# Kernel optimization log

Measured on AMD Instinct MI355X. Metric: run time of the kernel, lower is better.

The kernel has to match this reference:

```python
import jax, jax.numpy as jnp
import numpy as np

N_NODES = 50000
N_EDGES = 600000
N_GRAPHS = 256
N_FL1, N_MPL, N_FL2, N_FL3 = 128, 128, 128, 64
EPS = 1e-12


def _glorot(key, shape):
    lim = float(np.sqrt(6.0 / (shape[0] + shape[1])))
    return jax.random.uniform(key, shape, jnp.float32, -lim, lim)


def setup_inputs() -> dict:
    key = jax.random.key(0)
    ks = jax.random.split(key, 16)
    x = jax.random.normal(ks[0], (N_NODES, 5), jnp.float32)
    edge_index = jax.random.randint(ks[1], (2, N_EDGES), 0, N_NODES, jnp.int64)
    batch = jnp.sort(jax.random.randint(ks[2], (N_NODES,), 0, N_GRAPHS, jnp.int64))
    return {
        "x": x,
        "edge_index": edge_index,
        "batch": batch,
        "W_pre": _glorot(ks[3], (5, N_FL1)),
        "b_pre": jnp.zeros((N_FL1,), jnp.float32),
        "W1_l": _glorot(ks[4], (N_FL1, N_MPL)),
        "b1": jnp.zeros((N_MPL,), jnp.float32),
        "W1_r": _glorot(ks[5], (N_FL1, N_MPL)),
        "W2_l": _glorot(ks[6], (N_MPL, N_MPL)),
        "b2": jnp.zeros((N_MPL,), jnp.float32),
        "W2_r": _glorot(ks[7], (N_MPL, N_MPL)),
        "W_p1": _glorot(ks[8], (N_MPL, N_FL2)),
        "b_p1": jnp.zeros((N_FL2,), jnp.float32),
        "W_p2": _glorot(ks[9], (N_FL2, N_FL3)),
        "b_p2": jnp.zeros((N_FL3,), jnp.float32),
        "W_out": _glorot(ks[10], (N_FL3, 1)),
        "b_out": jnp.zeros((1,), jnp.float32),
    }


def _sage_conv(x, src, dst, deg_inv, W_l, b_l, W_r):
    # mean-aggregate neighbor messages x[src] onto dst, then linear transforms
    agg = jax.ops.segment_sum(x[src], dst, num_segments=N_NODES) * deg_inv  # [N, d]
    out = agg @ W_l + b_l + x @ W_r
    # normalize=True -> L2 normalize per node (PyG F.normalize, eps=1e-12)
    norm = jnp.sqrt(jnp.sum(out * out, axis=-1, keepdims=True))
    return out / jnp.maximum(norm, EPS)


def reference(x, edge_index, batch, W_pre, b_pre, W1_l, b1, W1_r,
              W2_l, b2, W2_r, W_p1, b_p1, W_p2, b_p2, W_out, b_out):
    src, dst = edge_index[0], edge_index[1]
    deg = jax.ops.segment_sum(jnp.ones((N_EDGES,), jnp.float32), dst, num_segments=N_NODES)
    deg_inv = (1.0 / jnp.maximum(deg, 1.0))[:, None]

    h = jax.nn.relu(x @ W_pre + b_pre)
    h = jax.nn.relu(_sage_conv(h, src, dst, deg_inv, W1_l, b1, W1_r))
    h = jax.nn.relu(_sage_conv(h, src, dst, deg_inv, W2_l, b2, W2_r))

    # global_mean_pool over graph ids in batch
    g_sum = jax.ops.segment_sum(h, batch, num_segments=N_GRAPHS)  # [G, d]
    g_cnt = jax.ops.segment_sum(jnp.ones((N_NODES,), jnp.float32), batch, num_segments=N_GRAPHS)
    g = g_sum / jnp.maximum(g_cnt, 1.0)[:, None]

    g = jax.nn.relu(g @ W_p1 + b_p1)
    g = jax.nn.relu(g @ W_p2 + b_p2)
    return g @ W_out + b_out  # [G, 1]
```

## Files before the change

kernel.cpp:

```cpp
#include <hip/hip_runtime.h>
#include <hip/hip_bf16.h>

#define N_NODES 50000
#define N_EDGES 600000
#define N_GRAPHS 256
#define D 128
#define NTILES 1563

typedef __bf16 bf16x8 __attribute__((ext_vector_type(8)));
typedef float f32x16 __attribute__((ext_vector_type(16)));
typedef unsigned short u16x8 __attribute__((ext_vector_type(8)));
typedef unsigned short u16x4 __attribute__((ext_vector_type(4)));

__device__ __forceinline__ float bf2f(unsigned short u) {
    unsigned v = ((unsigned)u) << 16;
    return __builtin_bit_cast(float, v);
}
__device__ __forceinline__ unsigned short f2bf(float f) {
    unsigned x = __builtin_bit_cast(unsigned, f);
    unsigned r = (x + 0x7fffu + ((x >> 16) & 1u)) >> 16;
    return (unsigned short)r;
}


#define ZERO_N (50048 + 32768)
#define ZERO_BLOCKS 324
#define PACK_BLOCKS 256
#define PRE_BLOCKS 3125

__global__ __launch_bounds__(256) void init_kernel(
    int* __restrict__ deg_gsum,
    const float* __restrict__ Wl1, const float* __restrict__ Wr1,
    const float* __restrict__ Wl2, const float* __restrict__ Wr2,
    unsigned short* __restrict__ Wpk,
    const float* __restrict__ x, const float* __restrict__ Wpre,
    const float* __restrict__ bpre, unsigned short* __restrict__ h0) {
    int bb = blockIdx.x;
    if (bb < ZERO_BLOCKS) {
        int i = bb * 256 + threadIdx.x;
        if (i < ZERO_N) deg_gsum[i] = 0;
    } else if (bb < ZERO_BLOCKS + PACK_BLOCKS) {
        int tid = (bb - ZERO_BLOCKS) * 256 + threadIdx.x;
        int conv = tid >> 15;
        int e = tid & 32767;
        int j = e & 7, lane = (e >> 3) & 63, ct = (e >> 9) & 3, kt = e >> 11;
        int k = kt * 16 + (lane >> 5) * 8 + j;
        int col = (lane & 31) * 4 + ct;
        const float* Wl = conv ? Wl2 : Wl1;
        const float* Wr = conv ? Wr2 : Wr1;
        float v = (k < 128) ? Wl[k * 128 + col] : Wr[(k - 128) * 128 + col];
        Wpk[tid] = f2bf(v);
    } else {
        int idx = (bb - ZERO_BLOCKS - PACK_BLOCKS) * 256 + threadIdx.x;
        if (idx >= N_NODES * 16) return;
        int node = idx >> 4, j8 = (idx & 15) * 8;
        const float* xr = x + node * 5;
        float acc[8];
#pragma unroll
        for (int c = 0; c < 8; ++c) acc[c] = bpre[j8 + c];
#pragma unroll
        for (int k = 0; k < 5; ++k) {
            float xv = xr[k];
#pragma unroll
            for (int c = 0; c < 8; ++c) acc[c] += xv * Wpre[k * D + j8 + c];
        }
        u16x8 o;
#pragma unroll
        for (int c = 0; c < 8; ++c) o[c] = f2bf(fmaxf(acc[c], 0.f));
        *(u16x8*)&h0[(size_t)node * D + j8] = o;
    }
}


__global__ void deg_kernel(const int* __restrict__ dst, int* __restrict__ deg) {
    int e = blockIdx.x * 256 + threadIdx.x;
    if (e < N_EDGES) atomicAdd(&deg[dst[e]], 1);
}

__global__ __launch_bounds__(1024) void scan_blk_kernel(const int* __restrict__ deg,
                                                        int* __restrict__ partial,
                                                        int* __restrict__ bsum) {
    __shared__ int tmp[1024];
    int tid = threadIdx.x;
    int i = blockIdx.x * 1024 + tid;
    int v = (i < N_NODES) ? deg[i] : 0;
    tmp[tid] = v;
    __syncthreads();
    for (int off = 1; off < 1024; off <<= 1) {
        int add = (tid >= off) ? tmp[tid - off] : 0;
        __syncthreads();
        tmp[tid] += add;
        __syncthreads();
    }
    if (i < N_NODES) partial[i] = tmp[tid] - v;
    if (tid == 1023) bsum[blockIdx.x] = tmp[tid];
}

__global__ __launch_bounds__(256) void scan_fix_kernel(const int* __restrict__ partial,
                                                       const int* __restrict__ bsum,
                                                       const int* __restrict__ deg,
                                                       int* __restrict__ row_start,
                                                       int* __restrict__ cursor,
                                                       float* __restrict__ deg_inv) {
    __shared__ int boff_s;
    int bucket = (blockIdx.x * 256) >> 10;
    if (threadIdx.x < 64) {
        int l = threadIdx.x;
        int v = (l < bucket) ? bsum[l] : 0;
#pragma unroll
        for (int m = 32; m >= 1; m >>= 1) v += __shfl_xor(v, m);
        if (l == 0) boff_s = v;
    }
    __syncthreads();
    int i = blockIdx.x * 256 + threadIdx.x;
    if (i >= N_NODES) return;
    int dg = deg[i];
    int rs = partial[i] + boff_s;
    row_start[i] = rs;
    cursor[i] = rs;
    deg_inv[i] = 1.0f / fmaxf((float)dg, 1.0f);
    if (i == N_NODES - 1) row_start[N_NODES] = rs + dg;
}

__global__ void fill_kernel(const int* __restrict__ src, const int* __restrict__ dst,
                            int* __restrict__ cursor, int* __restrict__ csr_src) {
    int e = blockIdx.x * 256 + threadIdx.x;
    if (e < N_EDGES) {
        int slot = atomicAdd(&cursor[dst[e]], 1);
        csr_src[slot] = src[e];
    }
}


__global__ __launch_bounds__(256) void conv_kernel(const unsigned short* __restrict__ hin,
                                                   const int* __restrict__ row_start,
                                                   const int* __restrict__ csr_src,
                                                   const float* __restrict__ deg_inv,
                                                   const unsigned short* __restrict__ Wp,
                                                   const float* __restrict__ b,
                                                   unsigned short* __restrict__ hout) {
    int wg = blockIdx.x * 4 + (threadIdx.x >> 6);
    if (wg >= NTILES) return;
    int lane = threadIdx.x & 63;
    int l31 = lane & 31, hi = lane >> 5;
    int row0 = wg * 32;
    int rowg = row0 + l31;
    bool valid = rowg < N_NODES;
    int rowc = valid ? rowg : (N_NODES - 1);

    int s = valid ? row_start[rowg] : 0;
    int e = valid ? row_start[rowg + 1] : 0;
    float di = valid ? deg_inv[rowg] : 1.0f;

    float a[8][8];
#pragma unroll
    for (int kt = 0; kt < 8; ++kt)
#pragma unroll
        for (int j = 0; j < 8; ++j) a[kt][j] = 0.f;

    int i = s;
    for (; i + 1 < e; i += 2) {
        int c0 = csr_src[i];
        int c1 = csr_src[i + 1];
        const unsigned short* p0 = hin + (size_t)c0 * D + hi * 8;
        const unsigned short* p1 = hin + (size_t)c1 * D + hi * 8;
        bf16x8 v0[8], v1[8];
#pragma unroll
        for (int kt = 0; kt < 8; ++kt) {
            v0[kt] = *(const bf16x8*)(p0 + kt * 16);
            v1[kt] = *(const bf16x8*)(p1 + kt * 16);
        }
#pragma unroll
        for (int kt = 0; kt < 8; ++kt)
#pragma unroll
            for (int j = 0; j < 8; ++j) a[kt][j] += (float)v0[kt][j] + (float)v1[kt][j];
    }
    if (i < e) {
        int c0 = csr_src[i];
        const unsigned short* p0 = hin + (size_t)c0 * D + hi * 8;
#pragma unroll
        for (int kt = 0; kt < 8; ++kt) {
            bf16x8 v0 = *(const bf16x8*)(p0 + kt * 16);
#pragma unroll
            for (int j = 0; j < 8; ++j) a[kt][j] += (float)v0[j];
        }
    }

    bf16x8 afr[16];
#pragma unroll
    for (int kt = 0; kt < 8; ++kt) {
        u16x8 t;
#pragma unroll
        for (int j = 0; j < 8; ++j) t[j] = f2bf(a[kt][j] * di);
        afr[kt] = __builtin_bit_cast(bf16x8, t);
    }
    const unsigned short* hrow = hin + (size_t)rowc * D + hi * 8;
#pragma unroll
    for (int kt = 0; kt < 8; ++kt) afr[8 + kt] = *(const bf16x8*)(hrow + kt * 16);

    const unsigned short* wbase = Wp + lane * 8;
    f32x16 acc[4];
#pragma unroll
    for (int ct = 0; ct < 4; ++ct) acc[ct] = (f32x16)(0.0f);
#pragma unroll
    for (int kt = 0; kt < 16; ++kt) {
#pragma unroll
        for (int ct = 0; ct < 4; ++ct) {
            bf16x8 bfrag = *(const bf16x8*)(wbase + (kt * 4 + ct) * 512);
            acc[ct] = __builtin_amdgcn_mfma_f32_32x32x16_bf16(afr[kt], bfrag, acc[ct], 0, 0, 0);
        }
    }

    float4 b4 = *(const float4*)&b[l31 * 4];
    float bb[4] = {b4.x, b4.y, b4.z, b4.w};
#pragma unroll
    for (int r = 0; r < 16; ++r) {
        float v[4];
        float ss = 0.f;
#pragma unroll
        for (int ct = 0; ct < 4; ++ct) {
            v[ct] = acc[ct][r] + bb[ct];
            ss += v[ct] * v[ct];
        }
        ss += __shfl_xor(ss, 1);
        ss += __shfl_xor(ss, 2);
        ss += __shfl_xor(ss, 4);
        ss += __shfl_xor(ss, 8);
        ss += __shfl_xor(ss, 16);
        float sc = 1.0f / fmaxf(sqrtf(ss), 1e-12f);
        int row = row0 + (r & 3) + 8 * (r >> 2) + 4 * hi;
        if (row < N_NODES) {
            u16x4 o;
#pragma unroll
            for (int ct = 0; ct < 4; ++ct) o[ct] = f2bf(fmaxf(v[ct] * sc, 0.f));
            *(u16x4*)(hout + (size_t)row * D + l31 * 4) = o;
        }
    }
}


__global__ __launch_bounds__(128) void pool_sum_kernel(const unsigned short* __restrict__ h,
                                                       const int* __restrict__ batch,
                                                       float* __restrict__ gsum) {
    int j = threadIdx.x;
    int i0 = blockIdx.x * 128;
    int i1 = i0 + 128;
    if (i1 > N_NODES) i1 = N_NODES;
    __shared__ int bids[128];
    if (i0 + j < N_NODES) bids[j] = batch[i0 + j];
    __syncthreads();
    float acc = 0.f;
    int cur = bids[0];
    for (int i = i0; i < i1; ++i) {
        int bid = bids[i - i0];
        if (bid != cur) {
            atomicAdd(&gsum[cur * D + j], acc);
            acc = 0.f;
            cur = bid;
        }
        acc += bf2f(h[(size_t)i * D + j]);
    }
    atomicAdd(&gsum[cur * D + j], acc);
}


__global__ __launch_bounds__(128) void mlp_kernel(const float* __restrict__ gsum,
                                                  const int* __restrict__ batch,
                                                  const float* __restrict__ Wp1,
                                                  const float* __restrict__ bp1,
                                                  const float* __restrict__ Wp2,
                                                  const float* __restrict__ bp2,
                                                  const float* __restrict__ Wout,
                                                  const float* __restrict__ bout,
                                                  float* __restrict__ out) {
    __shared__ float gin[128], y1[128], y2[64];
    __shared__ float cnt_s;
    int gid = blockIdx.x, j = threadIdx.x;
    if (j == 0) {
        int lo = 0, hi = N_NODES;
        while (lo < hi) { int m = (lo + hi) >> 1; if (batch[m] < gid) lo = m + 1; else hi = m; }
        int start = lo;
        lo = start; hi = N_NODES;
        while (lo < hi) { int m = (lo + hi) >> 1; if (batch[m] < gid + 1) lo = m + 1; else hi = m; }
        cnt_s = fmaxf((float)(lo - start), 1.0f);
    }
    __syncthreads();
    gin[j] = gsum[gid * 128 + j] / cnt_s;
    __syncthreads();
    float a = bp1[j];
    for (int k = 0; k < 128; ++k) a += gin[k] * Wp1[k * 128 + j];
    y1[j] = fmaxf(a, 0.f);
    __syncthreads();
    if (j < 64) {
        float a2 = bp2[j];
        for (int k = 0; k < 128; ++k) a2 += y1[k] * Wp2[k * 64 + j];
        y2[j] = fmaxf(a2, 0.f);
    }
    __syncthreads();
    if (j < 64) {
        float v = y2[j] * Wout[j];
#pragma unroll
        for (int m = 32; m >= 1; m >>= 1) v += __shfl_xor(v, m);
        if (j == 0) out[gid] = v + bout[0];
    }
}


extern "C" void kernel_launch(void* const* d_in, const int* in_sizes, int n_in,
                              void* d_out, int out_size, void* d_ws, size_t ws_size,
                              hipStream_t stream) {
    const float* x     = (const float*)d_in[0];
    const int*   ei    = (const int*)d_in[1];
    const int*   batch = (const int*)d_in[2];
    const float* W_pre = (const float*)d_in[3];
    const float* b_pre = (const float*)d_in[4];
    const float* W1_l  = (const float*)d_in[5];
    const float* b1    = (const float*)d_in[6];
    const float* W1_r  = (const float*)d_in[7];
    const float* W2_l  = (const float*)d_in[8];
    const float* b2    = (const float*)d_in[9];
    const float* W2_r  = (const float*)d_in[10];
    const float* W_p1  = (const float*)d_in[11];
    const float* b_p1  = (const float*)d_in[12];
    const float* W_p2  = (const float*)d_in[13];
    const float* b_p2  = (const float*)d_in[14];
    const float* W_out = (const float*)d_in[15];
    const float* b_out = (const float*)d_in[16];

    const int* src = ei;
    const int* dst = ei + N_EDGES;

    size_t off = 0;
    auto carve = [&](size_t bytes) {
        void* p = (char*)d_ws + off;
        off += (bytes + 255) & ~(size_t)255;
        return p;
    };
    int* deg       = (int*)carve(50048 * 4 + 32768 * 4);
    float* gsum    = (float*)(deg + 50048);
    int* row_start = (int*)carve((N_NODES + 1) * 4);
    int* cursor    = (int*)carve(N_NODES * 4);
    int* csr_src   = (int*)carve(N_EDGES * 4);
    float* deg_inv = (float*)carve(N_NODES * 4);
    int* partial   = (int*)carve(N_NODES * 4);
    int* bsum      = (int*)carve(64 * 4);
    unsigned short* h0 = (unsigned short*)carve((size_t)N_NODES * D * 2);
    unsigned short* h1 = (unsigned short*)carve((size_t)N_NODES * D * 2);
    unsigned short* Wp = (unsigned short*)carve(65536 * 2);
    unsigned short* h2 = h0;
    float* out = (float*)d_out;

    const int nblk_scan = (N_NODES + 1023) / 1024;

    init_kernel<<<ZERO_BLOCKS + PACK_BLOCKS + PRE_BLOCKS, 256, 0, stream>>>(
        deg, W1_l, W1_r, W2_l, W2_r, Wp, x, W_pre, b_pre, h0);

    deg_kernel<<<(N_EDGES + 255) / 256, 256, 0, stream>>>(dst, deg);
    scan_blk_kernel<<<nblk_scan, 1024, 0, stream>>>(deg, partial, bsum);
    scan_fix_kernel<<<(N_NODES + 255) / 256, 256, 0, stream>>>(partial, bsum, deg,
                                                               row_start, cursor, deg_inv);
    fill_kernel<<<(N_EDGES + 255) / 256, 256, 0, stream>>>(src, dst, cursor, csr_src);

    conv_kernel<<<(NTILES + 3) / 4, 256, 0, stream>>>(h0, row_start, csr_src, deg_inv,
                                                      Wp, b1, h1);
    conv_kernel<<<(NTILES + 3) / 4, 256, 0, stream>>>(h1, row_start, csr_src, deg_inv,
                                                      Wp + 32768, b2, h2);

    pool_sum_kernel<<<(N_NODES + 127) / 128, 128, 0, stream>>>(h2, batch, gsum);
    mlp_kernel<<<N_GRAPHS, 128, 0, stream>>>(gsum, batch, W_p1, b_p1, W_p2, b_p2,
                                             W_out, b_out, out);
}
```

Measured before the change: 229.9 us.

## Split SAGE conv into coalesced gather kernel and MFMA linear kernel, fuse pooling

The fused conv kernel, where each lane gathered a whole neighbor row, is split in two. A separate aggregation kernel uses 16 lanes per node with 8-way unrolled neighbor loads, and an MFMA linear kernel reads the aggregated bf16 features back from a new buffer. The second layer's linear kernel also performs global mean-pool summation through shared-memory partial sums and atomics, which removes the separate pool kernel. This gives better gather parallelism and memory coalescing, at the cost of an extra round trip through global memory for the aggregated features and extra launches.

```diff
diff --git a/kernel.cpp b/kernel.cpp
--- a/kernel.cpp
+++ b/kernel.cpp
@@ -132,87 +132,90 @@
 }
 
 
-__global__ __launch_bounds__(256) void conv_kernel(const unsigned short* __restrict__ hin,
-                                                   const int* __restrict__ row_start,
-                                                   const int* __restrict__ csr_src,
-                                                   const float* __restrict__ deg_inv,
-                                                   const unsigned short* __restrict__ Wp,
-                                                   const float* __restrict__ b,
-                                                   unsigned short* __restrict__ hout) {
+__global__ __launch_bounds__(256) void agg_kernel(const unsigned short* __restrict__ h,
+                                                  const int* __restrict__ row_start,
+                                                  const int* __restrict__ csr_src,
+                                                  const float* __restrict__ deg_inv,
+                                                  unsigned short* __restrict__ aggb) {
+    int node = blockIdx.x * 16 + (threadIdx.x >> 4);
+    int fl = threadIdx.x & 15;
+    if (node >= N_NODES) return;
+    int s = row_start[node], e = row_start[node + 1];
+    float a[8] = {0.f, 0.f, 0.f, 0.f, 0.f, 0.f, 0.f, 0.f};
+    int i = s;
+    for (; i + 7 < e; i += 8) {
+        int c[8];
+#pragma unroll
+        for (int q = 0; q < 8; ++q) c[q] = csr_src[i + q];
+        bf16x8 v[8];
+#pragma unroll
+        for (int q = 0; q < 8; ++q) v[q] = *(const bf16x8*)(h + (size_t)c[q] * D + fl * 8);
+#pragma unroll
+        for (int q = 0; q < 8; ++q)
+#pragma unroll
+            for (int j = 0; j < 8; ++j) a[j] += (float)v[q][j];
+    }
+    for (; i + 3 < e; i += 4) {
+        int c[4];
+#pragma unroll
+        for (int q = 0; q < 4; ++q) c[q] = csr_src[i + q];
+        bf16x8 v[4];
+#pragma unroll
+        for (int q = 0; q < 4; ++q) v[q] = *(const bf16x8*)(h + (size_t)c[q] * D + fl * 8);
+#pragma unroll
+        for (int q = 0; q < 4; ++q)
+#pragma unroll
+            for (int j = 0; j < 8; ++j) a[j] += (float)v[q][j];
+    }
+    for (; i < e; ++i) {
+        int c0 = csr_src[i];
+        bf16x8 v0 = *(const bf16x8*)(h + (size_t)c0 * D + fl * 8);
+#pragma unroll
+        for (int j = 0; j < 8; ++j) a[j] += (float)v0[j];
+    }
+    float di = deg_inv[node];
+    u16x8 o;
+#pragma unroll
+    for (int j = 0; j < 8; ++j) o[j] = f2bf(a[j] * di);
+    *(u16x8*)(aggb + (size_t)node * D + fl * 8) = o;
+}
+
+
+__global__ __launch_bounds__(256) void lin_mfma_kernel(const unsigned short* __restrict__ hin,
+                                                       const unsigned short* __restrict__ aggb,
+                                                       const unsigned short* __restrict__ Wp,
+                                                       const float* __restrict__ b,
+                                                       unsigned short* __restrict__ hout) {
     int wg = blockIdx.x * 4 + (threadIdx.x >> 6);
     if (wg >= NTILES) return;
     int lane = threadIdx.x & 63;
     int l31 = lane & 31, hi = lane >> 5;
     int row0 = wg * 32;
     int rowg = row0 + l31;
-    bool valid = rowg < N_NODES;
-    int rowc = valid ? rowg : (N_NODES - 1);
-
-    int s = valid ? row_start[rowg] : 0;
-    int e = valid ? row_start[rowg + 1] : 0;
-    float di = valid ? deg_inv[rowg] : 1.0f;
-
-    float a[8][8];
-#pragma unroll
-    for (int kt = 0; kt < 8; ++kt)
-#pragma unroll
-        for (int j = 0; j < 8; ++j) a[kt][j] = 0.f;
-
-    int i = s;
-    for (; i + 1 < e; i += 2) {
-        int c0 = csr_src[i];
-        int c1 = csr_src[i + 1];
-        const unsigned short* p0 = hin + (size_t)c0 * D + hi * 8;
-        const unsigned short* p1 = hin + (size_t)c1 * D + hi * 8;
-        bf16x8 v0[8], v1[8];
-#pragma unroll
-        for (int kt = 0; kt < 8; ++kt) {
-            v0[kt] = *(const bf16x8*)(p0 + kt * 16);
-            v1[kt] = *(const bf16x8*)(p1 + kt * 16);
-        }
-#pragma unroll
-        for (int kt = 0; kt < 8; ++kt)
-#pragma unroll
-            for (int j = 0; j < 8; ++j) a[kt][j] += (float)v0[kt][j] + (float)v1[kt][j];
-    }
-    if (i < e) {
-        int c0 = csr_src[i];
-        const unsigned short* p0 = hin + (size_t)c0 * D + hi * 8;
-#pragma unroll
-        for (int kt = 0; kt < 8; ++kt) {
-            bf16x8 v0 = *(const bf16x8*)(p0 + kt * 16);
-#pragma unroll
-            for (int j = 0; j < 8; ++j) a[kt][j] += (float)v0[j];
-        }
-    }
-
-    bf16x8 afr[16];
-#pragma unroll
-    for (int kt = 0; kt < 8; ++kt) {
-        u16x8 t;
-#pragma unroll
-        for (int j = 0; j < 8; ++j) t[j] = f2bf(a[kt][j] * di);
-        afr[kt] = __builtin_bit_cast(bf16x8, t);
-    }
-    const unsigned short* hrow = hin + (size_t)rowc * D + hi * 8;
-#pragma unroll
-    for (int kt = 0; kt < 8; ++kt) afr[8 + kt] = *(const bf16x8*)(hrow + kt * 16);
-
+    if (rowg > N_NODES - 1) rowg = N_NODES - 1;
+
+    const unsigned short* arow = aggb + (size_t)rowg * D + hi * 8;
+    const unsigned short* hrow = hin + (size_t)rowg * D + hi * 8;
     const unsigned short* wbase = Wp + lane * 8;
+
     f32x16 acc[4];
 #pragma unroll
     for (int ct = 0; ct < 4; ++ct) acc[ct] = (f32x16)(0.0f);
+
 #pragma unroll
     for (int kt = 0; kt < 16; ++kt) {
+        const unsigned short* asrc = (kt < 8) ? (arow + kt * 16) : (hrow + (kt - 8) * 16);
+        bf16x8 af = *(const bf16x8*)asrc;
 #pragma unroll
         for (int ct = 0; ct < 4; ++ct) {
             bf16x8 bfrag = *(const bf16x8*)(wbase + (kt * 4 + ct) * 512);
-            acc[ct] = __builtin_amdgcn_mfma_f32_32x32x16_bf16(afr[kt], bfrag, acc[ct], 0, 0, 0);
+            acc[ct] = __builtin_amdgcn_mfma_f32_32x32x16_bf16(af, bfrag, acc[ct], 0, 0, 0);
         }
     }
 
     float4 b4 = *(const float4*)&b[l31 * 4];
     float bb[4] = {b4.x, b4.y, b4.z, b4.w};
+
 #pragma unroll
     for (int r = 0; r < 16; ++r) {
         float v[4];
@@ -239,28 +242,91 @@
 }
 
 
-__global__ __launch_bounds__(128) void pool_sum_kernel(const unsigned short* __restrict__ h,
+__global__ __launch_bounds__(256) void lin_pool_kernel(const unsigned short* __restrict__ hin,
+                                                       const unsigned short* __restrict__ aggb,
+                                                       const unsigned short* __restrict__ Wp,
+                                                       const float* __restrict__ b,
                                                        const int* __restrict__ batch,
                                                        float* __restrict__ gsum) {
-    int j = threadIdx.x;
-    int i0 = blockIdx.x * 128;
-    int i1 = i0 + 128;
-    if (i1 > N_NODES) i1 = N_NODES;
-    __shared__ int bids[128];
-    if (i0 + j < N_NODES) bids[j] = batch[i0 + j];
-    __syncthreads();
-    float acc = 0.f;
-    int cur = bids[0];
-    for (int i = i0; i < i1; ++i) {
-        int bid = bids[i - i0];
-        if (bid != cur) {
-            atomicAdd(&gsum[cur * D + j], acc);
-            acc = 0.f;
-            cur = bid;
-        }
-        acc += bf2f(h[(size_t)i * D + j]);
-    }
-    atomicAdd(&gsum[cur * D + j], acc);
+    __shared__ float part[8][D];
+    __shared__ int gmin_s;
+    int t = threadIdx.x;
+#pragma unroll
+    for (int q = 0; q < 8; ++q) part[q][(t + q * 256) & 1023 & 127] = 0.f;
+    for (int q = t; q < 8 * D; q += 256) ((float*)part)[q] = 0.f;
+    if (t == 0) gmin_s = batch[blockIdx.x * 128];
+    __syncthreads();
+
+    int wg = blockIdx.x * 4 + (t >> 6);
+    bool wvalid = wg < NTILES;
+    int lane = t & 63;
+    int l31 = lane & 31, hi = lane >> 5;
+    int row0 = wg * 32;
+    int rowg = row0 + l31;
+    int rowc = (wvalid && rowg < N_NODES) ? rowg : (N_NODES - 1);
+
+    const unsigned short* arow = aggb + (size_t)rowc * D + hi * 8;
+    const unsigned short* hrow = hin + (size_t)rowc * D + hi * 8;
+    const unsigned short* wbase = Wp + lane * 8;
+
+    f32x16 acc[4];
+#pragma unroll
+    for (int ct = 0; ct < 4; ++ct) acc[ct] = (f32x16)(0.0f);
+
+#pragma unroll
+    for (int kt = 0; kt < 16; ++kt) {
+        const unsigned short* asrc = (kt < 8) ? (arow + kt * 16) : (hrow + (kt - 8) * 16);
+        bf16x8 af = *(const bf16x8*)asrc;
+#pragma unroll
+        for (int ct = 0; ct < 4; ++ct) {
+            bf16x8 bfrag = *(const bf16x8*)(wbase + (kt * 4 + ct) * 512);
+            acc[ct] = __builtin_amdgcn_mfma_f32_32x32x16_bf16(af, bfrag, acc[ct], 0, 0, 0);
+        }
+    }
+
+    float4 b4 = *(const float4*)&b[l31 * 4];
+    float bb[4] = {b4.x, b4.y, b4.z, b4.w};
+    int gmin = gmin_s;
+
+#pragma unroll
+    for (int r = 0; r < 16; ++r) {
+        float v[4];
+        float ss = 0.f;
+#pragma unroll
+        for (int ct = 0; ct < 4; ++ct) {
+            v[ct] = acc[ct][r] + bb[ct];
+            ss += v[ct] * v[ct];
+        }
+        ss += __shfl_xor(ss, 1);
+        ss += __shfl_xor(ss, 2);
+        ss += __shfl_xor(ss, 4);
+        ss += __shfl_xor(ss, 8);
+        ss += __shfl_xor(ss, 16);
+        float sc = 1.0f / fmaxf(sqrtf(ss), 1e-12f);
+        int row = row0 + (r & 3) + 8 * (r >> 2) + 4 * hi;
+        if (wvalid && row < N_NODES) {
+            int g = batch[row];
+            int gi = g - gmin;
+            if (gi < 8) {
+#pragma unroll
+                for (int ct = 0; ct < 4; ++ct)
+                    atomicAdd(&part[gi][l31 * 4 + ct], fmaxf(v[ct] * sc, 0.f));
+            } else {
+#pragma unroll
+                for (int ct = 0; ct < 4; ++ct)
+                    atomicAdd(&gsum[g * D + l31 * 4 + ct], fmaxf(v[ct] * sc, 0.f));
+            }
+        }
+    }
+
+    __syncthreads();
+    for (int q = t; q < 8 * D; q += 256) {
+        float val = ((float*)part)[q];
+        if (val != 0.f) {
+            int gi = q >> 7, c = q & 127;
+            atomicAdd(&gsum[(gmin + gi) * D + c], val);
+        }
+    }
 }
 
 
@@ -344,10 +410,10 @@
     float* deg_inv = (float*)carve(N_NODES * 4);
     int* partial   = (int*)carve(N_NODES * 4);
     int* bsum      = (int*)carve(64 * 4);
-    unsigned short* h0 = (unsigned short*)carve((size_t)N_NODES * D * 2);
-    unsigned short* h1 = (unsigned short*)carve((size_t)N_NODES * D * 2);
-    unsigned short* Wp = (unsigned short*)carve(65536 * 2);
-    unsigned short* h2 = h0;
+    unsigned short* h0   = (unsigned short*)carve((size_t)N_NODES * D * 2);
+    unsigned short* h1   = (unsigned short*)carve((size_t)N_NODES * D * 2);
+    unsigned short* aggb = (unsigned short*)carve((size_t)N_NODES * D * 2);
+    unsigned short* Wp   = (unsigned short*)carve(65536 * 2);
     float* out = (float*)d_out;
 
     const int nblk_scan = (N_NODES + 1023) / 1024;
@@ -361,12 +427,13 @@
                                                                row_start, cursor, deg_inv);
     fill_kernel<<<(N_EDGES + 255) / 256, 256, 0, stream>>>(src, dst, cursor, csr_src);
 
-    conv_kernel<<<(NTILES + 3) / 4, 256, 0, stream>>>(h0, row_start, csr_src, deg_inv,
-                                                      Wp, b1, h1);
-    conv_kernel<<<(NTILES + 3) / 4, 256, 0, stream>>>(h1, row_start, csr_src, deg_inv,
-                                                      Wp + 32768, b2, h2);
-
-    pool_sum_kernel<<<(N_NODES + 127) / 128, 128, 0, stream>>>(h2, batch, gsum);
+    agg_kernel<<<(N_NODES + 15) / 16, 256, 0, stream>>>(h0, row_start, csr_src, deg_inv, aggb);
+    lin_mfma_kernel<<<(NTILES + 3) / 4, 256, 0, stream>>>(h0, aggb, Wp, b1, h1);
+
+    agg_kernel<<<(N_NODES + 15) / 16, 256, 0, stream>>>(h1, row_start, csr_src, deg_inv, aggb);
+    lin_pool_kernel<<<(NTILES + 3) / 4, 256, 0, stream>>>(h1, aggb, Wp + 32768, b2,
+                                                          batch, gsum);
+
     mlp_kernel<<<N_GRAPHS, 128, 0, stream>>>(gsum, batch, W_p1, b_p1, W_p2, b_p2,
                                              W_out, b_out, out);
 }
```

New measurement: 213.4 us. 1.08x faster.

## Split SAGE conv into a gather-aggregation kernel and a column-split MFMA linear kernel

Applied to the files above, without the earlier changes.

Replaces the fused conv kernel, where each lane gathered a whole neighbor row for its own destination node, with two kernels. The first aggregates mean neighbor features using 16 lanes per node, with coalesced 16-byte gathers unrolled 8 edges deep. The second does the linear transform with four waves per 32-row tile, each wave owning 32 output columns, and combines the per-row L2 norms through shared memory. The repacked weight layout matches the new column split. This trades an extra bf16 round trip of the aggregate through global memory and two more launches for better gather parallelism and fewer registers per wave.

```diff
diff --git a/kernel.cpp b/kernel.cpp
--- a/kernel.cpp
+++ b/kernel.cpp
@@ -10,7 +10,6 @@
 typedef __bf16 bf16x8 __attribute__((ext_vector_type(8)));
 typedef float f32x16 __attribute__((ext_vector_type(16)));
 typedef unsigned short u16x8 __attribute__((ext_vector_type(8)));
-typedef unsigned short u16x4 __attribute__((ext_vector_type(4)));
 
 __device__ __forceinline__ float bf2f(unsigned short u) {
     unsigned v = ((unsigned)u) << 16;
@@ -45,7 +44,7 @@
         int e = tid & 32767;
         int j = e & 7, lane = (e >> 3) & 63, ct = (e >> 9) & 3, kt = e >> 11;
         int k = kt * 16 + (lane >> 5) * 8 + j;
-        int col = (lane & 31) * 4 + ct;
+        int col = ct * 32 + (lane & 31);
         const float* Wl = conv ? Wl2 : Wl1;
         const float* Wr = conv ? Wr2 : Wr1;
         float v = (k < 128) ? Wl[k * 128 + col] : Wr[(k - 128) * 128 + col];
@@ -132,108 +131,106 @@
 }
 
 
-__global__ __launch_bounds__(256) void conv_kernel(const unsigned short* __restrict__ hin,
-                                                   const int* __restrict__ row_start,
-                                                   const int* __restrict__ csr_src,
-                                                   const float* __restrict__ deg_inv,
-                                                   const unsigned short* __restrict__ Wp,
-                                                   const float* __restrict__ b,
-                                                   unsigned short* __restrict__ hout) {
-    int wg = blockIdx.x * 4 + (threadIdx.x >> 6);
-    if (wg >= NTILES) return;
-    int lane = threadIdx.x & 63;
+__global__ __launch_bounds__(256) void agg_kernel(const unsigned short* __restrict__ h,
+                                                  const int* __restrict__ row_start,
+                                                  const int* __restrict__ csr_src,
+                                                  const float* __restrict__ deg_inv,
+                                                  unsigned short* __restrict__ aggb) {
+    int node = blockIdx.x * 16 + (threadIdx.x >> 4);
+    int fl = threadIdx.x & 15;
+    if (node >= N_NODES) return;
+    int s = row_start[node], e = row_start[node + 1];
+    float a[8] = {0.f, 0.f, 0.f, 0.f, 0.f, 0.f, 0.f, 0.f};
+    int i = s;
+    for (; i + 7 < e; i += 8) {
+        int c[8];
+#pragma unroll
+        for (int q = 0; q < 8; ++q) c[q] = csr_src[i + q];
+        bf16x8 v[8];
+#pragma unroll
+        for (int q = 0; q < 8; ++q) v[q] = *(const bf16x8*)(h + (size_t)c[q] * D + fl * 8);
+#pragma unroll
+        for (int q = 0; q < 8; ++q)
+#pragma unroll
+            for (int j = 0; j < 8; ++j) a[j] += (float)v[q][j];
+    }
+    for (; i + 3 < e; i += 4) {
+        int c[4];
+#pragma unroll
+        for (int q = 0; q < 4; ++q) c[q] = csr_src[i + q];
+        bf16x8 v[4];
+#pragma unroll
+        for (int q = 0; q < 4; ++q) v[q] = *(const bf16x8*)(h + (size_t)c[q] * D + fl * 8);
+#pragma unroll
+        for (int q = 0; q < 4; ++q)
+#pragma unroll
+            for (int j = 0; j < 8; ++j) a[j] += (float)v[q][j];
+    }
+    for (; i < e; ++i) {
+        int c0 = csr_src[i];
+        bf16x8 v0 = *(const bf16x8*)(h + (size_t)c0 * D + fl * 8);
+#pragma unroll
+        for (int j = 0; j < 8; ++j) a[j] += (float)v0[j];
+    }
+    float di = deg_inv[node];
+    u16x8 o;
+#pragma unroll
+    for (int j = 0; j < 8; ++j) o[j] = f2bf(a[j] * di);
+    *(u16x8*)(aggb + (size_t)node * D + fl * 8) = o;
+}
+
+
+__global__ __launch_bounds__(256) void lin_quad_kernel(const unsigned short* __restrict__ hin,
+                                                       const unsigned short* __restrict__ aggb,
+                                                       const unsigned short* __restrict__ Wp,
+                                                       const float* __restrict__ b,
+                                                       unsigned short* __restrict__ hout) {
+    __shared__ float ssp[32][4];
+    int t = threadIdx.x;
+    int w = t >> 6;
+    int lane = t & 63;
     int l31 = lane & 31, hi = lane >> 5;
-    int row0 = wg * 32;
+    int row0 = blockIdx.x * 32;
     int rowg = row0 + l31;
-    bool valid = rowg < N_NODES;
-    int rowc = valid ? rowg : (N_NODES - 1);
-
-    int s = valid ? row_start[rowg] : 0;
-    int e = valid ? row_start[rowg + 1] : 0;
-    float di = valid ? deg_inv[rowg] : 1.0f;
-
-    float a[8][8];
-#pragma unroll
-    for (int kt = 0; kt < 8; ++kt)
-#pragma unroll
-        for (int j = 0; j < 8; ++j) a[kt][j] = 0.f;
-
-    int i = s;
-    for (; i + 1 < e; i += 2) {
-        int c0 = csr_src[i];
-        int c1 = csr_src[i + 1];
-        const unsigned short* p0 = hin + (size_t)c0 * D + hi * 8;
-        const unsigned short* p1 = hin + (size_t)c1 * D + hi * 8;
-        bf16x8 v0[8], v1[8];
-#pragma unroll
-        for (int kt = 0; kt < 8; ++kt) {
-            v0[kt] = *(const bf16x8*)(p0 + kt * 16);
-            v1[kt] = *(const bf16x8*)(p1 + kt * 16);
-        }
-#pragma unroll
-        for (int kt = 0; kt < 8; ++kt)
-#pragma unroll
-            for (int j = 0; j < 8; ++j) a[kt][j] += (float)v0[kt][j] + (float)v1[kt][j];
-    }
-    if (i < e) {
-        int c0 = csr_src[i];
-        const unsigned short* p0 = hin + (size_t)c0 * D + hi * 8;
-#pragma unroll
-        for (int kt = 0; kt < 8; ++kt) {
-            bf16x8 v0 = *(const bf16x8*)(p0 + kt * 16);
-#pragma unroll
-            for (int j = 0; j < 8; ++j) a[kt][j] += (float)v0[j];
-        }
-    }
-
-    bf16x8 afr[16];
-#pragma unroll
-    for (int kt = 0; kt < 8; ++kt) {
-        u16x8 t;
-#pragma unroll
-        for (int j = 0; j < 8; ++j) t[j] = f2bf(a[kt][j] * di);
-        afr[kt] = __builtin_bit_cast(bf16x8, t);
-    }
+    int rowc = (rowg < N_NODES) ? rowg : (N_NODES - 1);
+
+    const unsigned short* arow = aggb + (size_t)rowc * D + hi * 8;
     const unsigned short* hrow = hin + (size_t)rowc * D + hi * 8;
-#pragma unroll
-    for (int kt = 0; kt < 8; ++kt) afr[8 + kt] = *(const bf16x8*)(hrow + kt * 16);
-
-    const unsigned short* wbase = Wp + lane * 8;
-    f32x16 acc[4];
-#pragma unroll
-    for (int ct = 0; ct < 4; ++ct) acc[ct] = (f32x16)(0.0f);
+    const unsigned short* wbase = Wp + (size_t)w * 512 + lane * 8;
+
+    f32x16 acc = (f32x16)(0.0f);
 #pragma unroll
     for (int kt = 0; kt < 16; ++kt) {
-#pragma unroll
-        for (int ct = 0; ct < 4; ++ct) {
-            bf16x8 bfrag = *(const bf16x8*)(wbase + (kt * 4 + ct) * 512);
-            acc[ct] = __builtin_amdgcn_mfma_f32_32x32x16_bf16(afr[kt], bfrag, acc[ct], 0, 0, 0);
-        }
-    }
-
-    float4 b4 = *(const float4*)&b[l31 * 4];
-    float bb[4] = {b4.x, b4.y, b4.z, b4.w};
+        const unsigned short* asrc = (kt < 8) ? (arow + kt * 16) : (hrow + (kt - 8) * 16);
+        bf16x8 af = *(const bf16x8*)asrc;
+        bf16x8 bfrag = *(const bf16x8*)(wbase + kt * 2048);
+        acc = __builtin_amdgcn_mfma_f32_32x32x16_bf16(af, bfrag, acc, 0, 0, 0);
+    }
+
+    float bb = b[w * 32 + l31];
+
 #pragma unroll
     for (int r = 0; r < 16; ++r) {
-        float v[4];
-        float ss = 0.f;
-#pragma unroll
-        for (int ct = 0; ct < 4; ++ct) {
-            v[ct] = acc[ct][r] + bb[ct];
-            ss += v[ct] * v[ct];
-        }
+        float v = acc[r] + bb;
+        float ss = v * v;
         ss += __shfl_xor(ss, 1);
         ss += __shfl_xor(ss, 2);
         ss += __shfl_xor(ss, 4);
         ss += __shfl_xor(ss, 8);
         ss += __shfl_xor(ss, 16);
+        if (l31 == 0) ssp[(r & 3) + 8 * (r >> 2) + 4 * hi][w] = ss;
+    }
+    __syncthreads();
+
+#pragma unroll
+    for (int r = 0; r < 16; ++r) {
+        int rl = (r & 3) + 8 * (r >> 2) + 4 * hi;
+        float ss = ssp[rl][0] + ssp[rl][1] + ssp[rl][2] + ssp[rl][3];
         float sc = 1.0f / fmaxf(sqrtf(ss), 1e-12f);
-        int row = row0 + (r & 3) + 8 * (r >> 2) + 4 * hi;
+        int row = row0 + rl;
         if (row < N_NODES) {
-            u16x4 o;
-#pragma unroll
-            for (int ct = 0; ct < 4; ++ct) o[ct] = f2bf(fmaxf(v[ct] * sc, 0.f));
-            *(u16x4*)(hout + (size_t)row * D + l31 * 4) = o;
+            float v = (acc[r] + bb) * sc;
+            hout[(size_t)row * D + w * 32 + l31] = f2bf(fmaxf(v, 0.f));
         }
     }
 }
@@ -344,9 +341,10 @@
     float* deg_inv = (float*)carve(N_NODES * 4);
     int* partial   = (int*)carve(N_NODES * 4);
     int* bsum      = (int*)carve(64 * 4);
-    unsigned short* h0 = (unsigned short*)carve((size_t)N_NODES * D * 2);
-    unsigned short* h1 = (unsigned short*)carve((size_t)N_NODES * D * 2);
-    unsigned short* Wp = (unsigned short*)carve(65536 * 2);
+    unsigned short* h0   = (unsigned short*)carve((size_t)N_NODES * D * 2);
+    unsigned short* h1   = (unsigned short*)carve((size_t)N_NODES * D * 2);
+    unsigned short* aggb = (unsigned short*)carve((size_t)N_NODES * D * 2);
+    unsigned short* Wp   = (unsigned short*)carve(65536 * 2);
     unsigned short* h2 = h0;
     float* out = (float*)d_out;
 
@@ -361,10 +359,11 @@
                                                                row_start, cursor, deg_inv);
     fill_kernel<<<(N_EDGES + 255) / 256, 256, 0, stream>>>(src, dst, cursor, csr_src);
 
-    conv_kernel<<<(NTILES + 3) / 4, 256, 0, stream>>>(h0, row_start, csr_src, deg_inv,
-                                                      Wp, b1, h1);
-    conv_kernel<<<(NTILES + 3) / 4, 256, 0, stream>>>(h1, row_start, csr_src, deg_inv,
-                                                      Wp + 32768, b2, h2);
+    agg_kernel<<<(N_NODES + 15) / 16, 256, 0, stream>>>(h0, row_start, csr_src, deg_inv, aggb);
+    lin_quad_kernel<<<NTILES, 256, 0, stream>>>(h0, aggb, Wp, b1, h1);
+
+    agg_kernel<<<(N_NODES + 15) / 16, 256, 0, stream>>>(h1, row_start, csr_src, deg_inv, aggb);
+    lin_quad_kernel<<<NTILES, 256, 0, stream>>>(h1, aggb, Wp + 32768, b2, h2);
 
     pool_sum_kernel<<<(N_NODES + 127) / 128, 128, 0, stream>>>(h2, batch, gsum);
     mlp_kernel<<<N_GRAPHS, 128, 0, stream>>>(gsum, batch, W_p1, b_p1, W_p2, b_p2,
```

Measured after the change: 228.6 us. About the same (-0.6%).
